# Kernel tuning notes

Measured on AMD Instinct MI355X. Metric: run time of the kernel, lower is better.

The kernel has to match this reference:

```python
import jax, jax.numpy as jnp
import numpy as np

EMB = 1024
HEADS = 16
HEAD_DIM = EMB // HEADS
EPS = 1e-5


def setup_inputs() -> dict:
    key = jax.random.key(0)
    ks = jax.random.split(key, 10)
    B, T, D = 2, 2048, EMB
    s = 1.0 / np.sqrt(D)
    inp = {
        "x": jax.random.normal(ks[0], (B, T, D), dtype=jnp.float32),
        "wq": jax.random.normal(ks[1], (D, D), dtype=jnp.float32) * s,
        "bq": jnp.zeros((D,), jnp.float32),
        "wk": jax.random.normal(ks[2], (D, D), dtype=jnp.float32) * s,
        "bk": jnp.zeros((D,), jnp.float32),
        "wv": jax.random.normal(ks[3], (D, D), dtype=jnp.float32) * s,
        "bv": jnp.zeros((D,), jnp.float32),
        "wo": jax.random.normal(ks[4], (D, D), dtype=jnp.float32) * s,
        "bo": jnp.zeros((D,), jnp.float32),
        "gamma": jnp.ones((D,), jnp.float32),
        "beta": jnp.zeros((D,), jnp.float32),
    }
    return inp


def _attention(x, wq, bq, wk, bk, wv, bv, wo, bo, gamma, beta):
    B, T, D = x.shape
    H, Hd = HEADS, HEAD_DIM
    q = (x @ wq + bq).reshape(B, T, H, Hd)
    k = (x @ wk + bk).reshape(B, T, H, Hd)
    v = (x @ wv + bv).reshape(B, T, H, Hd)
    # scores: [B, H, T, T]
    scores = jnp.einsum("bthd,bshd->bhts", q, k) / np.sqrt(Hd)
    attn = jax.nn.softmax(scores, axis=-1)  # dropout is identity in eval
    ctx = jnp.einsum("bhts,bshd->bthd", attn, v).reshape(B, T, D)
    out = ctx @ wo + bo
    y = x + out  # residual (dropout identity)
    mu = jnp.mean(y, axis=-1, keepdims=True)
    var = jnp.var(y, axis=-1, keepdims=True)
    return (y - mu) * jax.lax.rsqrt(var + EPS) * gamma + beta


def reference(x, wq, bq, wk, bk, wv, bv, wo, bo, gamma, beta):
    return _attention(x, wq, bq, wk, bk, wv, bv, wo, bo, gamma, beta)
```

## Files before the change

kernel.cpp:

```cpp
#include <hip/hip_runtime.h>

#define BSZ   2
#define TSEQ  2048
#define DMOD  1024
#define NHEAD 16
#define HDIM  64
#define MROW  (BSZ*TSEQ)
#define LNEPS 1e-5f
#define QSCALE 0.125f

typedef __bf16 bf16x8 __attribute__((ext_vector_type(8)));
typedef float  f32x4  __attribute__((ext_vector_type(4)));
typedef unsigned short us8 __attribute__((ext_vector_type(8)));
typedef unsigned short us4 __attribute__((ext_vector_type(4)));

__device__ __forceinline__ unsigned short f2bf(float f) {
    unsigned u = __float_as_uint(f);
    u += 0x7FFF + ((u >> 16) & 1);
    return (unsigned short)(u >> 16);
}

__device__ __forceinline__ void gld_lds16(const void* g, void* l) {
    __builtin_amdgcn_global_load_lds(
        (const __attribute__((address_space(1))) unsigned int*)g,
        (__attribute__((address_space(3))) unsigned int*)l, 16, 0, 0);
}

__global__ __launch_bounds__(256) void cvtx_k(const float* __restrict__ x,
                                              unsigned short* __restrict__ Xb)
{
    const size_t i = ((size_t)blockIdx.x * 256 + threadIdx.x) * 8;
    float4 a = *(const float4*)&x[i];
    float4 b = *(const float4*)&x[i + 4];
    union { unsigned short u[8]; uint4 v; } o;
    o.u[0] = f2bf(a.x); o.u[1] = f2bf(a.y); o.u[2] = f2bf(a.z); o.u[3] = f2bf(a.w);
    o.u[4] = f2bf(b.x); o.u[5] = f2bf(b.y); o.u[6] = f2bf(b.z); o.u[7] = f2bf(b.w);
    *(uint4*)&Xb[i] = o.v;
}

__global__ __launch_bounds__(256) void wt_all_k(
    const float* __restrict__ wq, const float* __restrict__ wk,
    const float* __restrict__ wv, const float* __restrict__ wo,
    unsigned short* __restrict__ WqkvT, unsigned short* __restrict__ WoT)
{
    __shared__ float T[64][68];
    const int z = blockIdx.z;
    const float* W = (z == 0) ? wq : (z == 1) ? wk : (z == 2) ? wv : wo;
    unsigned short* Wt = (z < 3) ? (WqkvT + (size_t)z*1024*1024) : WoT;
    const int tid = threadIdx.x;
    const int bx = blockIdx.x, by = blockIdx.y;
    const int lr = tid >> 4, lc = (tid & 15) * 4;
    #pragma unroll
    for (int p = 0; p < 4; ++p) {
        const int kk = p*16 + lr;
        float4 v = *(const float4*)&W[(size_t)(by*64 + kk)*1024 + bx*64 + lc];
        T[lc+0][kk] = v.x; T[lc+1][kk] = v.y; T[lc+2][kk] = v.z; T[lc+3][kk] = v.w;
    }
    __syncthreads();
    #pragma unroll
    for (int p = 0; p < 2; ++p) {
        const int nl = p*32 + (tid >> 3);
        const int kb = (tid & 7) * 8;
        float4 a = *(const float4*)&T[nl][kb];
        float4 b = *(const float4*)&T[nl][kb+4];
        union { unsigned short u[8]; uint4 v; } o;
        o.u[0]=f2bf(a.x); o.u[1]=f2bf(a.y); o.u[2]=f2bf(a.z); o.u[3]=f2bf(a.w);
        o.u[4]=f2bf(b.x); o.u[5]=f2bf(b.y); o.u[6]=f2bf(b.z); o.u[7]=f2bf(b.w);
        *(uint4*)&Wt[(size_t)(bx*64 + nl)*1024 + by*64 + kb] = o.v;
    }
}

template<int MODE>
__global__ __launch_bounds__(256) void gemm_bf16_k(
    const unsigned short* __restrict__ A, const unsigned short* __restrict__ Bt,
    const float* __restrict__ b0, const float* __restrict__ b1,
    const float* __restrict__ b2,
    void* __restrict__ o0, void* __restrict__ o1, void* __restrict__ o2)
{
    __shared__ unsigned short As[128*32];
    __shared__ unsigned short Bs[128*32];
    const int tid  = threadIdx.x;
    const int wv   = tid >> 6;
    const int lane = tid & 63;
    const int quad = lane >> 4;
    const int l16  = lane & 15;
    const int wm   = wv & 1, wn = wv >> 1;
    const int bm = blockIdx.y * 128, bn = blockIdx.x * 128;

    const int r0 = lane >> 2;
    const int jb = lane & 3;
    const unsigned short* Ag[2]; const unsigned short* Bg[2];
    void *ldsA[2], *ldsB[2];
    #pragma unroll
    for (int j = 0; j < 2; ++j) {
        const int c = wv*2 + j;
        const int R = c*16 + r0;
        const int gb = (jb ^ ((R >> 1) & 3)) * 8;
        Ag[j] = A  + (size_t)(bm + R)*1024 + gb;
        Bg[j] = Bt + (size_t)(bn + R)*1024 + gb;
        ldsA[j] = (char*)As + c*1024;
        ldsB[j] = (char*)Bs + c*1024;
    }

    const int asw = (quad ^ ((l16 >> 1) & 3)) * 8;
    const unsigned short* ap[4]; const unsigned short* bp[4];
    #pragma unroll
    for (int t = 0; t < 4; ++t) {
        ap[t] = &As[(wm*64 + t*16 + l16)*32 + asw];
        bp[t] = &Bs[(wn*64 + t*16 + l16)*32 + asw];
    }

    f32x4 acc[4][4];
    #pragma unroll
    for (int i = 0; i < 4; ++i)
        #pragma unroll
        for (int j = 0; j < 4; ++j) acc[i][j] = (f32x4){0.f,0.f,0.f,0.f};

    for (int k0 = 0; k0 < 1024; k0 += 32) {
        __syncthreads();
        gld_lds16(Ag[0] + k0, ldsA[0]);
        gld_lds16(Ag[1] + k0, ldsA[1]);
        gld_lds16(Bg[0] + k0, ldsB[0]);
        gld_lds16(Bg[1] + k0, ldsB[1]);
        __syncthreads();
        bf16x8 af[4], bfr[4];
        #pragma unroll
        for (int t = 0; t < 4; ++t) {
            af[t]  = *(const bf16x8*)ap[t];
            bfr[t] = *(const bf16x8*)bp[t];
        }
        #pragma unroll
        for (int i = 0; i < 4; ++i)
            #pragma unroll
            for (int j = 0; j < 4; ++j)
                acc[i][j] = __builtin_amdgcn_mfma_f32_16x16x32_bf16(af[i], bfr[j], acc[i][j], 0, 0, 0);
    }

    if (MODE == 0) {
        float* C = (float*)o0;
        #pragma unroll
        for (int nt = 0; nt < 4; ++nt) {
            const int gcol = bn + wn*64 + nt*16 + l16;
            const float bs = b0[gcol];
            #pragma unroll
            for (int mt = 0; mt < 4; ++mt)
                #pragma unroll
                for (int r = 0; r < 4; ++r) {
                    const int grow = bm + wm*64 + mt*16 + quad*4 + r;
                    C[(size_t)grow*1024 + gcol] = acc[mt][nt][r] + bs;
                }
        }
    } else {
        const int seg = bn >> 10;
        const float* bias = (seg == 0) ? b0 : (seg == 1) ? b1 : b2;
        const int cb = bn & 1023;
        if (seg < 2) {
            unsigned short* O = (unsigned short*)((seg == 0) ? o0 : o1);
            const float sc = (seg == 0) ? QSCALE : 1.0f;
            #pragma unroll
            for (int nt = 0; nt < 4; ++nt) {
                const int col = cb + wn*64 + nt*16 + l16;
                const float bs = bias[col];
                #pragma unroll
                for (int mt = 0; mt < 4; ++mt)
                    #pragma unroll
                    for (int r = 0; r < 4; ++r) {
                        const int grow = bm + wm*64 + mt*16 + quad*4 + r;
                        O[(size_t)grow*1024 + col] = f2bf((acc[mt][nt][r] + bs) * sc);
                    }
            }
        } else {
            unsigned short* O = (unsigned short*)o2;
            #pragma unroll
            for (int nt = 0; nt < 4; ++nt) {
                const int ch = cb + wn*64 + nt*16 + l16;
                const float bs = bias[ch];
                #pragma unroll
                for (int mt = 0; mt < 4; ++mt) {
                    const int grow0 = bm + wm*64 + mt*16 + quad*4;
                    us4 o;
                    #pragma unroll
                    for (int r = 0; r < 4; ++r) o[r] = f2bf(acc[mt][nt][r] + bs);
                    *(us4*)&O[(size_t)ch*MROW + grow0] = o;
                }
            }
        }
    }
}

__global__ __launch_bounds__(256) void attn_k(
    const unsigned short* __restrict__ Qg,
    const unsigned short* __restrict__ Kg,
    const unsigned short* __restrict__ Vtg,
    unsigned short* __restrict__ CTX)
{
    __shared__ __align__(16) unsigned short Qs[128*72];
    __shared__ __align__(16) unsigned short Ks[128*64];
    __shared__ __align__(16) unsigned short Vs[64*128];

    const int tid  = threadIdx.x;
    const int wv   = tid >> 6;
    const int lane = tid & 63;
    const int quad = lane >> 4;
    const int l16  = lane & 15;
    const int qb   = blockIdx.x * 128;
    const int h    = blockIdx.y;
    const int b    = blockIdx.z;

    {
        const int r = tid >> 3, c = (tid & 7) * 8;
        const unsigned short* Qrow = Qg + ((size_t)(b*TSEQ + qb))*DMOD + h*HDIM;
        #pragma unroll
        for (int p = 0; p < 4; ++p)
            *(us8*)&Qs[(p*32 + r)*72 + c] =
                *(const us8*)&Qrow[(size_t)(p*32 + r)*DMOD + c];
    }
    __syncthreads();
    bf16x8 qf[2][2];
    #pragma unroll
    for (int nt = 0; nt < 2; ++nt)
        #pragma unroll
        for (int kh = 0; kh < 2; ++kh)
            qf[nt][kh] = *(const bf16x8*)&Qs[(wv*32 + nt*16 + l16)*72 + kh*32 + quad*8];

    f32x4 oacc[4][2];
    #pragma unroll
    for (int dt = 0; dt < 4; ++dt)
        #pragma unroll
        for (int nt = 0; nt < 2; ++nt) oacc[dt][nt] = (f32x4){0.f,0.f,0.f,0.f};
    float lsum[2] = {0.f, 0.f};

    const unsigned short* Kp = Kg  + ((size_t)(b*TSEQ))*DMOD + h*HDIM;
    const unsigned short* Vp = Vtg + ((size_t)(h*HDIM))*MROW + b*TSEQ;

    const int krow_l = tid >> 3;
    const int kjb    = tid & 7;
    const int vrow_l = tid >> 4;
    const int vjb    = tid & 15;

    const int pa_ = l16 >> 2, pb_ = l16 & 3;
    const int rowA_l = pa_*8 + pb_;
    const int swA = (rowA_l ^ (rowA_l >> 2)) & 7;
    const int rowB_l = rowA_l + 4;
    const int swB = (rowB_l ^ (rowB_l >> 2)) & 7;

    for (int it = 0; it < TSEQ/128; ++it) {
        const int kbase = it * 128;
        __syncthreads();
        #pragma unroll
        for (int p = 0; p < 4; ++p) {
            const int kr = p*32 + krow_l;
            const int kgb = (kjb ^ ((kr ^ (kr >> 2)) & 7)) * 8;
            gld_lds16(Kp + (size_t)(kbase + kr)*DMOD + kgb,
                      (char*)Ks + (p*32 + wv*8)*128);
            const int vr = p*16 + vrow_l;
            const int vgb = (vjb ^ (vr & 7)) * 8;
            gld_lds16(Vp + (size_t)vr*MROW + kbase + vgb,
                      (char*)Vs + (p*16 + wv*4)*256);
        }
        __syncthreads();

        #pragma unroll
        for (int g = 0; g < 4; ++g) {
            const int rA = g*32 + rowA_l;
            const int rB = g*32 + rowB_l;
            bf16x8 ka0 = *(const bf16x8*)&Ks[rA*64 + ((quad    ^ swA))*8];
            bf16x8 ka1 = *(const bf16x8*)&Ks[rA*64 + (((4+quad) ^ swA))*8];
            bf16x8 kb0 = *(const bf16x8*)&Ks[rB*64 + ((quad    ^ swB))*8];
            bf16x8 kb1 = *(const bf16x8*)&Ks[rB*64 + (((4+quad) ^ swB))*8];
            f32x4 sA[2], sB[2];
            #pragma unroll
            for (int nt = 0; nt < 2; ++nt) {
                f32x4 z = (f32x4){0.f,0.f,0.f,0.f};
                z = __builtin_amdgcn_mfma_f32_16x16x32_bf16(ka0, qf[nt][0], z, 0, 0, 0);
                sA[nt] = __builtin_amdgcn_mfma_f32_16x16x32_bf16(ka1, qf[nt][1], z, 0, 0, 0);
                z = (f32x4){0.f,0.f,0.f,0.f};
                z = __builtin_amdgcn_mfma_f32_16x16x32_bf16(kb0, qf[nt][0], z, 0, 0, 0);
                sB[nt] = __builtin_amdgcn_mfma_f32_16x16x32_bf16(kb1, qf[nt][1], z, 0, 0, 0);
            }

            bf16x8 pf[2];
            #pragma unroll
            for (int nt = 0; nt < 2; ++nt) {
                float eA[4], eB[4];
                #pragma unroll
                for (int r = 0; r < 4; ++r) { eA[r] = __expf(sA[nt][r]); eB[r] = __expf(sB[nt][r]); }
                lsum[nt] += ((eA[0]+eA[1]) + (eA[2]+eA[3])) + ((eB[0]+eB[1]) + (eB[2]+eB[3]));
                union { unsigned d[4]; bf16x8 v; } up;
                up.d[0] = __builtin_amdgcn_perm(__float_as_uint(eA[1]), __float_as_uint(eA[0]), 0x07060302);
                up.d[1] = __builtin_amdgcn_perm(__float_as_uint(eA[3]), __float_as_uint(eA[2]), 0x07060302);
                up.d[2] = __builtin_amdgcn_perm(__float_as_uint(eB[1]), __float_as_uint(eB[0]), 0x07060302);
                up.d[3] = __builtin_amdgcn_perm(__float_as_uint(eB[3]), __float_as_uint(eB[2]), 0x07060302);
                pf[nt] = up.v;
            }

            #pragma unroll
            for (int dt = 0; dt < 4; ++dt) {
                bf16x8 vf = *(const bf16x8*)
                    &Vs[(dt*16 + l16)*128 + (((g*4 + quad) ^ (l16 & 7)))*8];
                #pragma unroll
                for (int nt = 0; nt < 2; ++nt)
                    oacc[dt][nt] = __builtin_amdgcn_mfma_f32_16x16x32_bf16(
                        vf, pf[nt], oacc[dt][nt], 0, 0, 0);
            }
        }
    }

    #pragma unroll
    for (int nt = 0; nt < 2; ++nt) {
        float s = lsum[nt];
        s += __shfl_xor(s, 16, 64);
        s += __shfl_xor(s, 32, 64);
        const float inv = 1.f / s;
        const int q = qb + wv*32 + nt*16 + l16;
        unsigned short* crow = CTX + ((size_t)(b*TSEQ + q))*DMOD + h*HDIM;
        #pragma unroll
        for (int dt = 0; dt < 4; ++dt) {
            us4 o;
            #pragma unroll
            for (int r = 0; r < 4; ++r) o[r] = f2bf(oacc[dt][nt][r] * inv);
            *(us4*)&crow[dt*16 + quad*4] = o;
        }
    }
}

__global__ __launch_bounds__(256) void ln_k(
    const float* __restrict__ x, float* __restrict__ y,
    const float* __restrict__ gamma, const float* __restrict__ beta)
{
    __shared__ float rs[4], rss[4];
    const int row = blockIdx.x;
    const int tid = threadIdx.x;
    const int c = tid * 4;
    const float4 xv = *(const float4*)&x[(size_t)row*DMOD + c];
    const float4 pv = *(const float4*)&y[(size_t)row*DMOD + c];
    const float v0 = xv.x + pv.x, v1 = xv.y + pv.y;
    const float v2 = xv.z + pv.z, v3 = xv.w + pv.w;
    float s  = v0 + v1 + v2 + v3;
    float ss = v0*v0 + v1*v1 + v2*v2 + v3*v3;
    #pragma unroll
    for (int o = 32; o > 0; o >>= 1) {
        s  += __shfl_down(s,  o, 64);
        ss += __shfl_down(ss, o, 64);
    }
    if ((tid & 63) == 0) { rs[tid >> 6] = s; rss[tid >> 6] = ss; }
    __syncthreads();
    s  = rs[0] + rs[1] + rs[2] + rs[3];
    ss = rss[0] + rss[1] + rss[2] + rss[3];
    const float mean = s * (1.f/DMOD);
    const float var  = ss * (1.f/DMOD) - mean*mean;
    const float rstd = rsqrtf(var + LNEPS);
    const float4 gv = *(const float4*)&gamma[c];
    const float4 bv = *(const float4*)&beta[c];
    float4 o;
    o.x = (v0 - mean)*rstd*gv.x + bv.x;
    o.y = (v1 - mean)*rstd*gv.y + bv.y;
    o.z = (v2 - mean)*rstd*gv.z + bv.z;
    o.w = (v3 - mean)*rstd*gv.w + bv.w;
    *(float4*)&y[(size_t)row*DMOD + c] = o;
}

extern "C" void kernel_launch(void* const* d_in, const int* in_sizes, int n_in,
                              void* d_out, int out_size, void* d_ws, size_t ws_size,
                              hipStream_t stream) {
    const float* x     = (const float*)d_in[0];
    const float* wq    = (const float*)d_in[1];
    const float* bq    = (const float*)d_in[2];
    const float* wk    = (const float*)d_in[3];
    const float* bk    = (const float*)d_in[4];
    const float* wvp   = (const float*)d_in[5];
    const float* bvp   = (const float*)d_in[6];
    const float* wo    = (const float*)d_in[7];
    const float* bo    = (const float*)d_in[8];
    const float* gamma = (const float*)d_in[9];
    const float* beta  = (const float*)d_in[10];
    float* out = (float*)d_out;

    unsigned short* Xb    = (unsigned short*)d_ws;
    unsigned short* WqkvT = Xb    + (size_t)MROW*DMOD;
    unsigned short* WoT   = WqkvT + (size_t)3072*1024;
    unsigned short* Qb    = WoT   + (size_t)1024*1024;
    unsigned short* Kb    = Qb    + (size_t)MROW*DMOD;
    unsigned short* VtG   = Kb    + (size_t)MROW*DMOD;
    unsigned short* CTXb  = VtG   + (size_t)DMOD*MROW;

    cvtx_k<<<(MROW*DMOD)/(256*8), 256, 0, stream>>>(x, Xb);
    wt_all_k<<<dim3(16,16,4), 256, 0, stream>>>(wq, wk, wvp, wo, WqkvT, WoT);

    gemm_bf16_k<1><<<dim3(3072/128, MROW/128), 256, 0, stream>>>(
        Xb, WqkvT, bq, bk, bvp, Qb, Kb, VtG);

    attn_k<<<dim3(TSEQ/128, NHEAD, BSZ), 256, 0, stream>>>(Qb, Kb, VtG, CTXb);

    gemm_bf16_k<0><<<dim3(DMOD/128, MROW/128), 256, 0, stream>>>(
        CTXb, WoT, bo, bo, bo, out, nullptr, nullptr);

    ln_k<<<MROW, 256, 0, stream>>>(x, out, gamma, beta);
}
```

Baseline: 225.5 us.

## Split attention waves across key halves, use exp2 and MFMA row sums

Restructures the attention kernel so each wave handles 64 queries over one half of the key range, with the two key halves merged through LDS at the end. K and V tile loads are split by wave role, with precomputed offsets. The Q scale is folded with log2(e) so the exponent uses the native exp2 instruction. Row sums are computed with an MFMA against a ones vector instead of scalar adds and shuffles. The aim is more reuse of each loaded K/V fragment across query tiles and less VALU work per tile. The cost is more accumulator registers and an extra LDS reduction step.

```diff
diff --git a/kernel.cpp b/kernel.cpp
--- a/kernel.cpp
+++ b/kernel.cpp
@@ -7,7 +7,7 @@
 #define HDIM  64
 #define MROW  (BSZ*TSEQ)
 #define LNEPS 1e-5f
-#define QSCALE 0.125f
+#define QSCALE 0.18033688011f
 
 typedef __bf16 bf16x8 __attribute__((ext_vector_type(8)));
 typedef float  f32x4  __attribute__((ext_vector_type(4)));
@@ -18,6 +18,14 @@
     unsigned u = __float_as_uint(f);
     u += 0x7FFF + ((u >> 16) & 1);
     return (unsigned short)(u >> 16);
+}
+
+__device__ __forceinline__ float fexp2(float x) {
+#if __has_builtin(__builtin_amdgcn_exp2f)
+    return __builtin_amdgcn_exp2f(x);
+#else
+    return __expf(x * 0.6931471805599453f);
+#endif
 }
 
 __device__ __forceinline__ void gld_lds16(const void* g, void* l) {
@@ -188,138 +196,170 @@
     }
 }
 
-__global__ __launch_bounds__(256) void attn_k(
+__global__ __launch_bounds__(256, 2) void attn_k(
     const unsigned short* __restrict__ Qg,
     const unsigned short* __restrict__ Kg,
     const unsigned short* __restrict__ Vtg,
     unsigned short* __restrict__ CTX)
 {
-    __shared__ __align__(16) unsigned short Qs[128*72];
-    __shared__ __align__(16) unsigned short Ks[128*64];
-    __shared__ __align__(16) unsigned short Vs[64*128];
+    __shared__ __align__(16) char lds_raw[51200];
+    unsigned short* Qs = (unsigned short*)lds_raw;
+    unsigned short* Ks = (unsigned short*)(lds_raw + 18432);
+    unsigned short* Vs = (unsigned short*)(lds_raw + 34816);
+    float* Od = (float*)lds_raw;
+    float* Ld = (float*)(lds_raw + 34816);
 
     const int tid  = threadIdx.x;
     const int wv   = tid >> 6;
     const int lane = tid & 63;
     const int quad = lane >> 4;
     const int l16  = lane & 15;
+    const int wq   = wv & 1;
+    const int wk   = wv >> 1;
     const int qb   = blockIdx.x * 128;
     const int h    = blockIdx.y;
     const int b    = blockIdx.z;
 
     {
-        const int r = tid >> 3, c = (tid & 7) * 8;
-        const unsigned short* Qrow = Qg + ((size_t)(b*TSEQ + qb))*DMOD + h*HDIM;
-        #pragma unroll
-        for (int p = 0; p < 4; ++p)
-            *(us8*)&Qs[(p*32 + r)*72 + c] =
-                *(const us8*)&Qrow[(size_t)(p*32 + r)*DMOD + c];
+        const int row = tid & 127, cb = (tid >> 7) * 32;
+        const unsigned short* Qrow = Qg + ((size_t)(b*TSEQ + qb + row))*DMOD + h*HDIM + cb;
+        #pragma unroll
+        for (int j = 0; j < 4; ++j)
+            *(us8*)&Qs[row*72 + cb + j*8] = *(const us8*)&Qrow[j*8];
     }
     __syncthreads();
-    bf16x8 qf[2][2];
-    #pragma unroll
-    for (int nt = 0; nt < 2; ++nt)
+    bf16x8 qf[4][2];
+    #pragma unroll
+    for (int nt = 0; nt < 4; ++nt)
         #pragma unroll
         for (int kh = 0; kh < 2; ++kh)
-            qf[nt][kh] = *(const bf16x8*)&Qs[(wv*32 + nt*16 + l16)*72 + kh*32 + quad*8];
-
-    f32x4 oacc[4][2];
+            qf[nt][kh] = *(const bf16x8*)&Qs[(wq*64 + nt*16 + l16)*72 + kh*32 + quad*8];
+
+    const int sr = lane >> 3;
+    const int sc = lane & 7;
+    const bool isK = (wv < 2);
+    const int half = wv & 1;
+    const unsigned short* gbase;
+    unsigned int goff[8];
+    unsigned short* ldst;
+    if (isK) {
+        gbase = Kg + ((size_t)(b*TSEQ + half*1024))*DMOD + h*HDIM;
+        #pragma unroll
+        for (int s = 0; s < 8; ++s) {
+            const int R = s*8 + sr;
+            const int gc = sc ^ ((R ^ (R >> 2)) & 7);
+            goff[s] = (unsigned)(R*DMOD + gc*8);
+        }
+        ldst = Ks + half*4096;
+    } else {
+        gbase = Vtg + ((size_t)(h*HDIM))*MROW + b*TSEQ + half*1024;
+        #pragma unroll
+        for (int s = 0; s < 8; ++s) {
+            const int D = s*8 + sr;
+            const int gc = sc ^ (D & 7);
+            goff[s] = (unsigned)(D*MROW + gc*8);
+        }
+        ldst = Vs + half*4096;
+    }
+    const size_t gstep = isK ? (size_t)64*DMOD : (size_t)64;
+
+    const int rowA_l = (l16 >> 2)*8 + (l16 & 3);
+    const int rowB_l = rowA_l + 4;
+    const int swA = (rowA_l ^ (rowA_l >> 2)) & 7;
+    const int swB = (rowB_l ^ (rowB_l >> 2)) & 7;
+    const unsigned short* KsW = Ks + wk*4096;
+    const unsigned short* VsW = Vs + wk*4096;
+
+    bf16x8 onef;
+    { union { unsigned short u[8]; bf16x8 v; } o1;
+      #pragma unroll
+      for (int i = 0; i < 8; ++i) o1.u[i] = 0x3F80;
+      onef = o1.v; }
+
+    f32x4 oacc[4][4];
+    f32x4 lacc[4];
     #pragma unroll
     for (int dt = 0; dt < 4; ++dt)
         #pragma unroll
-        for (int nt = 0; nt < 2; ++nt) oacc[dt][nt] = (f32x4){0.f,0.f,0.f,0.f};
-    float lsum[2] = {0.f, 0.f};
-
-    const unsigned short* Kp = Kg  + ((size_t)(b*TSEQ))*DMOD + h*HDIM;
-    const unsigned short* Vp = Vtg + ((size_t)(h*HDIM))*MROW + b*TSEQ;
-
-    const int krow_l = tid >> 3;
-    const int kjb    = tid & 7;
-    const int vrow_l = tid >> 4;
-    const int vjb    = tid & 15;
-
-    const int pa_ = l16 >> 2, pb_ = l16 & 3;
-    const int rowA_l = pa_*8 + pb_;
-    const int swA = (rowA_l ^ (rowA_l >> 2)) & 7;
-    const int rowB_l = rowA_l + 4;
-    const int swB = (rowB_l ^ (rowB_l >> 2)) & 7;
-
-    for (int it = 0; it < TSEQ/128; ++it) {
-        const int kbase = it * 128;
+        for (int nt = 0; nt < 4; ++nt) oacc[dt][nt] = (f32x4){0.f,0.f,0.f,0.f};
+    #pragma unroll
+    for (int nt = 0; nt < 4; ++nt) lacc[nt] = (f32x4){0.f,0.f,0.f,0.f};
+
+    for (int it = 0; it < 16; ++it) {
         __syncthreads();
         #pragma unroll
-        for (int p = 0; p < 4; ++p) {
-            const int kr = p*32 + krow_l;
-            const int kgb = (kjb ^ ((kr ^ (kr >> 2)) & 7)) * 8;
-            gld_lds16(Kp + (size_t)(kbase + kr)*DMOD + kgb,
-                      (char*)Ks + (p*32 + wv*8)*128);
-            const int vr = p*16 + vrow_l;
-            const int vgb = (vjb ^ (vr & 7)) * 8;
-            gld_lds16(Vp + (size_t)vr*MROW + kbase + vgb,
-                      (char*)Vs + (p*16 + wv*4)*256);
-        }
+        for (int s = 0; s < 8; ++s)
+            gld_lds16(gbase + (size_t)it*gstep + goff[s], ldst + s*512);
         __syncthreads();
 
         #pragma unroll
-        for (int g = 0; g < 4; ++g) {
-            const int rA = g*32 + rowA_l;
-            const int rB = g*32 + rowB_l;
-            bf16x8 ka0 = *(const bf16x8*)&Ks[rA*64 + ((quad    ^ swA))*8];
-            bf16x8 ka1 = *(const bf16x8*)&Ks[rA*64 + (((4+quad) ^ swA))*8];
-            bf16x8 kb0 = *(const bf16x8*)&Ks[rB*64 + ((quad    ^ swB))*8];
-            bf16x8 kb1 = *(const bf16x8*)&Ks[rB*64 + (((4+quad) ^ swB))*8];
-            f32x4 sA[2], sB[2];
-            #pragma unroll
-            for (int nt = 0; nt < 2; ++nt) {
+        for (int gl = 0; gl < 2; ++gl) {
+            const int rA = gl*32 + rowA_l;
+            const int rB = gl*32 + rowB_l;
+            bf16x8 ka0 = *(const bf16x8*)&KsW[rA*64 + ((quad     ^ swA))*8];
+            bf16x8 ka1 = *(const bf16x8*)&KsW[rA*64 + (((4+quad) ^ swA))*8];
+            bf16x8 kb0 = *(const bf16x8*)&KsW[rB*64 + ((quad     ^ swB))*8];
+            bf16x8 kb1 = *(const bf16x8*)&KsW[rB*64 + (((4+quad) ^ swB))*8];
+            bf16x8 vf[4];
+            #pragma unroll
+            for (int dt = 0; dt < 4; ++dt)
+                vf[dt] = *(const bf16x8*)&VsW[(dt*16 + l16)*64 + ((gl*4 + quad) ^ (l16 & 7))*8];
+
+            #pragma unroll
+            for (int nt = 0; nt < 4; ++nt) {
                 f32x4 z = (f32x4){0.f,0.f,0.f,0.f};
                 z = __builtin_amdgcn_mfma_f32_16x16x32_bf16(ka0, qf[nt][0], z, 0, 0, 0);
-                sA[nt] = __builtin_amdgcn_mfma_f32_16x16x32_bf16(ka1, qf[nt][1], z, 0, 0, 0);
+                f32x4 sA = __builtin_amdgcn_mfma_f32_16x16x32_bf16(ka1, qf[nt][1], z, 0, 0, 0);
                 z = (f32x4){0.f,0.f,0.f,0.f};
                 z = __builtin_amdgcn_mfma_f32_16x16x32_bf16(kb0, qf[nt][0], z, 0, 0, 0);
-                sB[nt] = __builtin_amdgcn_mfma_f32_16x16x32_bf16(kb1, qf[nt][1], z, 0, 0, 0);
-            }
-
-            bf16x8 pf[2];
-            #pragma unroll
-            for (int nt = 0; nt < 2; ++nt) {
+                f32x4 sB = __builtin_amdgcn_mfma_f32_16x16x32_bf16(kb1, qf[nt][1], z, 0, 0, 0);
+
                 float eA[4], eB[4];
                 #pragma unroll
-                for (int r = 0; r < 4; ++r) { eA[r] = __expf(sA[nt][r]); eB[r] = __expf(sB[nt][r]); }
-                lsum[nt] += ((eA[0]+eA[1]) + (eA[2]+eA[3])) + ((eB[0]+eB[1]) + (eB[2]+eB[3]));
+                for (int r = 0; r < 4; ++r) { eA[r] = fexp2(sA[r]); eB[r] = fexp2(sB[r]); }
                 union { unsigned d[4]; bf16x8 v; } up;
                 up.d[0] = __builtin_amdgcn_perm(__float_as_uint(eA[1]), __float_as_uint(eA[0]), 0x07060302);
                 up.d[1] = __builtin_amdgcn_perm(__float_as_uint(eA[3]), __float_as_uint(eA[2]), 0x07060302);
                 up.d[2] = __builtin_amdgcn_perm(__float_as_uint(eB[1]), __float_as_uint(eB[0]), 0x07060302);
                 up.d[3] = __builtin_amdgcn_perm(__float_as_uint(eB[3]), __float_as_uint(eB[2]), 0x07060302);
-                pf[nt] = up.v;
+                const bf16x8 pf = up.v;
+
+                lacc[nt] = __builtin_amdgcn_mfma_f32_16x16x32_bf16(onef, pf, lacc[nt], 0, 0, 0);
+                #pragma unroll
+                for (int dt = 0; dt < 4; ++dt)
+                    oacc[dt][nt] = __builtin_amdgcn_mfma_f32_16x16x32_bf16(vf[dt], pf, oacc[dt][nt], 0, 0, 0);
             }
-
+        }
+    }
+
+    __syncthreads();
+    if (wk == 0) {
+        float* od = Od + wq*64*68;
+        #pragma unroll
+        for (int nt = 0; nt < 4; ++nt) {
+            #pragma unroll
+            for (int dt = 0; dt < 4; ++dt)
+                *(f32x4*)&od[(nt*16 + l16)*68 + dt*16 + quad*4] = oacc[dt][nt];
+            if (quad == 0) Ld[wq*64 + nt*16 + l16] = lacc[nt][0];
+        }
+    }
+    __syncthreads();
+    if (wk == 1) {
+        const float* od = Od + wq*64*68;
+        #pragma unroll
+        for (int nt = 0; nt < 4; ++nt) {
+            const float l = Ld[wq*64 + nt*16 + l16] + lacc[nt][0];
+            const float inv = 1.f / l;
+            const int q = qb + wq*64 + nt*16 + l16;
+            unsigned short* crow = CTX + ((size_t)(b*TSEQ + q))*DMOD + h*HDIM;
             #pragma unroll
             for (int dt = 0; dt < 4; ++dt) {
-                bf16x8 vf = *(const bf16x8*)
-                    &Vs[(dt*16 + l16)*128 + (((g*4 + quad) ^ (l16 & 7)))*8];
-                #pragma unroll
-                for (int nt = 0; nt < 2; ++nt)
-                    oacc[dt][nt] = __builtin_amdgcn_mfma_f32_16x16x32_bf16(
-                        vf, pf[nt], oacc[dt][nt], 0, 0, 0);
+                f32x4 p = *(const f32x4*)&od[(nt*16 + l16)*68 + dt*16 + quad*4];
+                us4 o;
+                #pragma unroll
+                for (int r = 0; r < 4; ++r) o[r] = f2bf((p[r] + oacc[dt][nt][r]) * inv);
+                *(us4*)&crow[dt*16 + quad*4] = o;
             }
-        }
-    }
-
-    #pragma unroll
-    for (int nt = 0; nt < 2; ++nt) {
-        float s = lsum[nt];
-        s += __shfl_xor(s, 16, 64);
-        s += __shfl_xor(s, 32, 64);
-        const float inv = 1.f / s;
-        const int q = qb + wv*32 + nt*16 + l16;
-        unsigned short* crow = CTX + ((size_t)(b*TSEQ + q))*DMOD + h*HDIM;
-        #pragma unroll
-        for (int dt = 0; dt < 4; ++dt) {
-            us4 o;
-            #pragma unroll
-            for (int r = 0; r < 4; ++r) o[r] = f2bf(oacc[dt][nt][r] * inv);
-            *(us4*)&crow[dt*16 + quad*4] = o;
         }
     }
 }
```

New measurement: 212.3 us. -5.8%, faster.
